# Kernel tuning notes

Measured on AMD Instinct MI355X. Metric: run time of the kernel, lower is better.

## Reference

```python
import jax, jax.numpy as jnp
import numpy as np

# BlockShuffle (butterfly) dims for in=4096 -> out=16384, nblocks=16
K, Q, P = 16, 256, 256   # w1: (k, q, p), k*p = n = 4096
L, S, R = 16, 1024, 256  # w2: (l, s, r), l*r = k*q = 4096; out = l*s = 16384
BATCH = 4096


def setup_inputs() -> dict:
    key = jax.random.key(0)
    kx, k1, k2 = jax.random.split(key, 3)
    x = jax.random.normal(kx, (BATCH, K * P), dtype=jnp.float32)
    # xavier-style init: std = fan_in^-0.5 (per _init_weights)
    w1 = jax.random.normal(k1, (K, Q, P), dtype=jnp.float32) * (P ** -0.5)
    w2 = jax.random.normal(k2, (L, S, R), dtype=jnp.float32) * (R ** -0.5)
    return {"x": x, "w1": w1, "w2": w2}


def reference(x, w1, w2):
    bd, n = x.shape
    k, q, p = w1.shape
    l, s, r = w2.shape
    # stage 1: block-diagonal matmul over k blocks of size p -> q
    out1 = jnp.einsum('bkp,kqp->bkq', x.reshape(bd, k, p), w1)  # (bd, k, q)
    # shuffle: view (k*q) as (r, l), transpose -> (l, r) blocks
    out1 = out1.reshape(bd, r, l).transpose(0, 2, 1)            # (bd, l, r)
    # stage 2: block-diagonal matmul over l blocks of size r -> s;
    # torch permute(1,2,0).reshape gives index order i = s_idx * l + l_idx
    out2 = jnp.einsum('blr,lsr->bsl', out1, w2)                 # (bd, s, l)
    return out2.reshape(bd, s * l)
```

## Files before the change

kernel.cpp:

```cpp
#include <hip/hip_runtime.h>

typedef __attribute__((ext_vector_type(8)))  short short8;
typedef __attribute__((ext_vector_type(4)))  short short4v;
typedef __attribute__((ext_vector_type(4)))  float f32x4;
typedef __attribute__((ext_vector_type(16))) float f32x16;

__device__ inline short f2bf(float f) {
  unsigned u = __float_as_uint(f);
  u += 0x7fffu + ((u >> 16) & 1u);
  return (short)(u >> 16);
}

__device__ __forceinline__ void barrier_lgkm() {
  asm volatile("s_waitcnt lgkmcnt(0)" ::: "memory");
  __builtin_amdgcn_s_barrier();
}

__global__ void cvt_all(const float* __restrict__ w1, short* __restrict__ w1b,
                        const float* __restrict__ w2, short* __restrict__ w2f) {
  if (blockIdx.x < 1024) {
    int i = blockIdx.x * 256 + threadIdx.x;
    f32x4 v = ((const f32x4*)w1)[i];
    short4v o;
    o[0] = f2bf(v[0]); o[1] = f2bf(v[1]); o[2] = f2bf(v[2]); o[3] = f2bf(v[3]);
    ((short4v*)w1b)[i] = o;
    return;
  }
  int t = (blockIdx.x - 1024) * 256 + threadIdx.x;
  int lane  = t & 63;
  int f     = t >> 6;
  int kh    = f & 1;
  int ck    = (f >> 1) & 7;
  int stile = (f >> 4) & 31;
  int l     = f >> 9;
  int lrow = lane & 31, khalf = lane >> 5;
  int s = stile * 32 + lrow;
  int r = ck * 32 + kh * 16 + khalf * 8;
  const float* src = w2 + (size_t)(l * 1024 + s) * 256 + r;
  f32x4 lo = *(const f32x4*)src;
  f32x4 hi = *(const f32x4*)(src + 4);
  short8 o;
  o[0]=f2bf(lo[0]); o[1]=f2bf(lo[1]); o[2]=f2bf(lo[2]); o[3]=f2bf(lo[3]);
  o[4]=f2bf(hi[0]); o[5]=f2bf(hi[1]); o[6]=f2bf(hi[2]); o[7]=f2bf(hi[3]);
  ((short8*)w2f)[t] = o;
}

__global__ __launch_bounds__(256) void stage1_kernel(
    const float* __restrict__ x, const short* __restrict__ w1b, short* __restrict__ interf) {
  __shared__ __align__(16) char smem[65536];
  const int tid  = threadIdx.x;
  const int lane = tid & 63;
  const int wq   = tid >> 6;
  const int b0   = blockIdx.x * 64;
  const int k    = blockIdx.y;
  const int q0w  = wq * 64;
  const int lr   = lane & 15;
  const int kid  = lane >> 4;

  #pragma unroll
  for (int i = 0; i < 16; ++i) {
    int idx = i * 256 + tid;
    int row = idx >> 6, seg = idx & 63;
    f32x4 v = *(const f32x4*)(x + (size_t)(b0 + row) * 4096 + k * 256 + seg * 4);
    int byte = (row * 1024 + seg * 16) ^ ((row & 7) << 4);
    *(f32x4*)(smem + byte) = v;
  }
  barrier_lgkm();

  f32x4 acc[4][4] = {};
  const short* wbase = w1b + k * 65536 + (q0w + lr) * 256 + kid * 8;

  #pragma unroll
  for (int kk = 0; kk < 256; kk += 32) {
    short8 a[4], b[4];
    #pragma unroll
    for (int mt = 0; mt < 4; ++mt) {
      int row = mt * 16 + lr;
      int u = row * 1024 + kid * 32 + kk * 4;
      int s = (row & 7) << 4;
      f32x4 lo = *(const f32x4*)(smem + (u ^ s));
      f32x4 hi = *(const f32x4*)(smem + ((u + 16) ^ s));
      short8 av;
      av[0] = f2bf(lo[0]); av[1] = f2bf(lo[1]); av[2] = f2bf(lo[2]); av[3] = f2bf(lo[3]);
      av[4] = f2bf(hi[0]); av[5] = f2bf(hi[1]); av[6] = f2bf(hi[2]); av[7] = f2bf(hi[3]);
      a[mt] = av;
    }
    #pragma unroll
    for (int nt = 0; nt < 4; ++nt)
      b[nt] = *(const short8*)(wbase + nt * 16 * 256 + kk);
    #pragma unroll
    for (int mt = 0; mt < 4; ++mt)
      #pragma unroll
      for (int nt = 0; nt < 4; ++nt)
        acc[mt][nt] = __builtin_amdgcn_mfma_f32_16x16x32_bf16(a[mt], b[nt], acc[mt][nt], 0, 0, 0);
  }

  barrier_lgkm();

  #pragma unroll
  for (int mt = 0; mt < 4; ++mt) {
    #pragma unroll
    for (int j = 0; j < 4; ++j) {
      int blocal = mt * 16 + kid * 4 + j;
      int byte = (blocal * 512 + lr * 32 + wq * 8) ^ ((blocal & 7) << 4);
      short4v v;
      #pragma unroll
      for (int nt = 0; nt < 4; ++nt) v[nt] = f2bf(acc[mt][nt][j]);
      *(short4v*)(smem + byte) = v;
    }
  }
  barrier_lgkm();

  const int brow = lane & 31, khalf = lane >> 5;
  #pragma unroll
  for (int j = 0; j < 8; ++j) {
    int f   = j * 4 + wq;
    int btl = f >> 4, l = f & 15;
    int blc = btl * 32 + brow;
    int rbyte = (blc * 512 + l * 32 + khalf * 16) ^ ((blc & 7) << 4);
    short8 v = *(const short8*)(smem + rbyte);
    size_t off = (((size_t)(blockIdx.x * 2 + btl) * 16 + l) * 16 + k) * 512 + lane * 8;
    *(short8*)(interf + off) = v;
  }
}

__global__ __launch_bounds__(1024) void stage2_kernel(
    const short* __restrict__ interf, const short* __restrict__ w2f, float* __restrict__ out) {
  __shared__ float clds[16 * 1024];
  const int tid  = threadIdx.x;
  const int lane = tid & 63;
  const int l    = tid >> 6;
  const int lrow = lane & 31;
  const int khalf = lane >> 5;

  const int L    = blockIdx.x;
  const int xcd  = L & 7;
  const int pos  = L >> 3;
  const int pass = pos >> 6;
  const int idx  = pos & 63;
  const int bt   = idx & 3;
  const int st   = idx >> 2;
  const int BBT  = xcd * 8 + pass * 4 + bt;
  const int BST  = st;
  const int b0 = BBT * 64, s0 = BST * 64;

  const short* ap = interf + (size_t)(BBT * 2) * 131072 + l * 8192 + lane * 8;
  const short* bp = w2f + (size_t)l * 262144 + (size_t)(BST * 2) * 8192 + lane * 8;

  f32x16 acc[2][2] = {};

  #pragma unroll
  for (int ks = 0; ks < 16; ++ks) {
    short8 a0 = *(const short8*)(ap + ks * 512);
    short8 a1 = *(const short8*)(ap + 131072 + ks * 512);
    short8 b0v = *(const short8*)(bp + ks * 512);
    short8 b1v = *(const short8*)(bp + 8192 + ks * 512);
    acc[0][0] = __builtin_amdgcn_mfma_f32_32x32x16_bf16(a0, b0v, acc[0][0], 0, 0, 0);
    acc[0][1] = __builtin_amdgcn_mfma_f32_32x32x16_bf16(a0, b1v, acc[0][1], 0, 0, 0);
    acc[1][0] = __builtin_amdgcn_mfma_f32_32x32x16_bf16(a1, b0v, acc[1][0], 0, 0, 0);
    acc[1][1] = __builtin_amdgcn_mfma_f32_32x32x16_bf16(a1, b1v, acc[1][1], 0, 0, 0);
  }

  #pragma unroll
  for (int c = 0; c < 4; ++c) {
    const int bt2 = c >> 1, rh = c & 1;
    #pragma unroll
    for (int stt = 0; stt < 2; ++stt) {
      int scol = stt * 32 + lrow;
      #pragma unroll
      for (int rr = 0; rr < 8; ++rr) {
        int row16 = (rr & 3) + 8 * (rr >> 2) + 4 * khalf;
        int colx = scol * 16 + (l ^ ((scol & 3) << 2) ^ (((row16 >> 2) & 3) << 2));
        clds[row16 * 1024 + colx] = acc[bt2][stt][rh * 8 + rr];
      }
    }
    barrier_lgkm();
    #pragma unroll
    for (int p = 0; p < 4; ++p) {
      int idx2 = p * 1024 + tid;
      int row  = idx2 >> 8;
      int slot = idx2 & 255;
      int scol = slot >> 2, lq = slot & 3;
      int colx = scol * 16 + ((lq * 4) ^ ((scol & 3) << 2) ^ (((row >> 2) & 3) << 2));
      f32x4 v = *(const f32x4*)&clds[row * 1024 + colx];
      __builtin_nontemporal_store(
          v, (f32x4*)(out + (size_t)(b0 + c * 16 + row) * 16384
                          + (size_t)(s0 + scol) * 16 + lq * 4));
    }
    barrier_lgkm();
  }
}

extern "C" void kernel_launch(void* const* d_in, const int* in_sizes, int n_in,
                              void* d_out, int out_size, void* d_ws, size_t ws_size,
                              hipStream_t stream) {
  const float* x  = (const float*)d_in[0];
  const float* w1 = (const float*)d_in[1];
  const float* w2 = (const float*)d_in[2];
  float* out = (float*)d_out;

  short* interf = (short*)d_ws;
  short* w1b    = (short*)((char*)d_ws + (32u << 20));
  short* w2f    = (short*)((char*)d_ws + (34u << 20));

  cvt_all<<<3072, 256, 0, stream>>>(w1, w1b, w2, w2f);
  stage1_kernel<<<dim3(64, 16), 256, 0, stream>>>(x, w1b, interf);
  stage2_kernel<<<1024, 1024, 0, stream>>>(interf, w2f, out);
}
```

Measured before the change: 133.5 us.

## Fuse weight conversion into stage1 and read fp32 w1 directly

Removes the separate cvt_all kernel launch. The w2 bf16 repack now runs as a prologue inside stage1, with each of the 1024 blocks converting 512 entries. w1 is now read as fp32 and converted to bf16 inline in the MFMA loop, rather than read from a pre-converted buffer. This saves one launch and one pass over the weights, but doubles the bytes stage1 reads for w1 and adds conversion ALU work in the inner loop, repeated across the 64 batch blocks.

```diff
diff --git a/kernel.cpp b/kernel.cpp
--- a/kernel.cpp
+++ b/kernel.cpp
@@ -16,37 +16,10 @@
   __builtin_amdgcn_s_barrier();
 }
 
-__global__ void cvt_all(const float* __restrict__ w1, short* __restrict__ w1b,
-                        const float* __restrict__ w2, short* __restrict__ w2f) {
-  if (blockIdx.x < 1024) {
-    int i = blockIdx.x * 256 + threadIdx.x;
-    f32x4 v = ((const f32x4*)w1)[i];
-    short4v o;
-    o[0] = f2bf(v[0]); o[1] = f2bf(v[1]); o[2] = f2bf(v[2]); o[3] = f2bf(v[3]);
-    ((short4v*)w1b)[i] = o;
-    return;
-  }
-  int t = (blockIdx.x - 1024) * 256 + threadIdx.x;
-  int lane  = t & 63;
-  int f     = t >> 6;
-  int kh    = f & 1;
-  int ck    = (f >> 1) & 7;
-  int stile = (f >> 4) & 31;
-  int l     = f >> 9;
-  int lrow = lane & 31, khalf = lane >> 5;
-  int s = stile * 32 + lrow;
-  int r = ck * 32 + kh * 16 + khalf * 8;
-  const float* src = w2 + (size_t)(l * 1024 + s) * 256 + r;
-  f32x4 lo = *(const f32x4*)src;
-  f32x4 hi = *(const f32x4*)(src + 4);
-  short8 o;
-  o[0]=f2bf(lo[0]); o[1]=f2bf(lo[1]); o[2]=f2bf(lo[2]); o[3]=f2bf(lo[3]);
-  o[4]=f2bf(hi[0]); o[5]=f2bf(hi[1]); o[6]=f2bf(hi[2]); o[7]=f2bf(hi[3]);
-  ((short8*)w2f)[t] = o;
-}
-
 __global__ __launch_bounds__(256) void stage1_kernel(
-    const float* __restrict__ x, const short* __restrict__ w1b, short* __restrict__ interf) {
+    const float* __restrict__ x, const float* __restrict__ w1,
+    const float* __restrict__ w2, short* __restrict__ interf,
+    short* __restrict__ w2f) {
   __shared__ __align__(16) char smem[65536];
   const int tid  = threadIdx.x;
   const int lane = tid & 63;
@@ -57,6 +30,30 @@
   const int lr   = lane & 15;
   const int kid  = lane >> 4;
 
+  {
+    int flat = blockIdx.y * 64 + blockIdx.x;
+    #pragma unroll
+    for (int i = 0; i < 2; ++i) {
+      int t = flat * 512 + i * 256 + tid;
+      int lane2  = t & 63;
+      int f      = t >> 6;
+      int kh     = f & 1;
+      int ck     = (f >> 1) & 7;
+      int stile  = (f >> 4) & 31;
+      int l      = f >> 9;
+      int lrow2 = lane2 & 31, khalf2 = lane2 >> 5;
+      int s = stile * 32 + lrow2;
+      int r = ck * 32 + kh * 16 + khalf2 * 8;
+      const float* src = w2 + (size_t)(l * 1024 + s) * 256 + r;
+      f32x4 lo = *(const f32x4*)src;
+      f32x4 hi = *(const f32x4*)(src + 4);
+      short8 o;
+      o[0]=f2bf(lo[0]); o[1]=f2bf(lo[1]); o[2]=f2bf(lo[2]); o[3]=f2bf(lo[3]);
+      o[4]=f2bf(hi[0]); o[5]=f2bf(hi[1]); o[6]=f2bf(hi[2]); o[7]=f2bf(hi[3]);
+      ((short8*)w2f)[t] = o;
+    }
+  }
+
   #pragma unroll
   for (int i = 0; i < 16; ++i) {
     int idx = i * 256 + tid;
@@ -68,7 +65,7 @@
   barrier_lgkm();
 
   f32x4 acc[4][4] = {};
-  const short* wbase = w1b + k * 65536 + (q0w + lr) * 256 + kid * 8;
+  const float* wbase = w1 + k * 65536 + (q0w + lr) * 256 + kid * 8;
 
   #pragma unroll
   for (int kk = 0; kk < 256; kk += 32) {
@@ -86,8 +83,15 @@
       a[mt] = av;
     }
     #pragma unroll
-    for (int nt = 0; nt < 4; ++nt)
-      b[nt] = *(const short8*)(wbase + nt * 16 * 256 + kk);
+    for (int nt = 0; nt < 4; ++nt) {
+      const float* bp8 = wbase + nt * 16 * 256 + kk;
+      f32x4 blo = *(const f32x4*)bp8;
+      f32x4 bhi = *(const f32x4*)(bp8 + 4);
+      short8 bv;
+      bv[0] = f2bf(blo[0]); bv[1] = f2bf(blo[1]); bv[2] = f2bf(blo[2]); bv[3] = f2bf(blo[3]);
+      bv[4] = f2bf(bhi[0]); bv[5] = f2bf(bhi[1]); bv[6] = f2bf(bhi[2]); bv[7] = f2bf(bhi[3]);
+      b[nt] = bv;
+    }
     #pragma unroll
     for (int mt = 0; mt < 4; ++mt)
       #pragma unroll
@@ -200,10 +204,8 @@
   float* out = (float*)d_out;
 
   short* interf = (short*)d_ws;
-  short* w1b    = (short*)((char*)d_ws + (32u << 20));
   short* w2f    = (short*)((char*)d_ws + (34u << 20));
 
-  cvt_all<<<3072, 256, 0, stream>>>(w1, w1b, w2, w2f);
-  stage1_kernel<<<dim3(64, 16), 256, 0, stream>>>(x, w1b, interf);
+  stage1_kernel<<<dim3(64, 16), 256, 0, stream>>>(x, w1, w2, interf, w2f);
   stage2_kernel<<<1024, 1024, 0, stream>>>(interf, w2f, out);
 }
```

New measurement: 142.6 us. 1.07x slower.
